# Kernel optimization log

Hardware: AMD Instinct MI355X
Metric: run time of the kernel (lower is better)

## Reference

```python
import jax, jax.numpy as jnp
import numpy as np

NC, NP, H, E, EL = 4096, 8192, 128, 500000, 500000


def setup_inputs() -> dict:
    key = jax.random.key(0)
    ks = jax.random.split(key, 32)
    W = lambda i, shape: jax.random.normal(ks[i], shape, dtype=jnp.float32) * 0.02
    inp = {
        "x_country": jax.random.normal(ks[0], (NC, NC), dtype=jnp.float32),
        "x_product": jax.random.normal(ks[1], (NP, NP), dtype=jnp.float32),
        # input projections (Linear(num_x, hidden)) and node-id embeddings
        "Wc_lin": W(2, (NC, H)), "bc_lin": jnp.zeros((H,), jnp.float32),
        "Wp_lin": W(3, (NP, H)), "bp_lin": jnp.zeros((H,), jnp.float32),
        "emb_c": W(4, (NC, H)),
        "emb_p": W(5, (NP, H)),
        # SAGEConv params per layer per edge type (lin_l has bias, lin_r does not)
        "W1ep_l": W(6, (H, H)), "b1ep": jnp.zeros((H,), jnp.float32), "W1ep_r": W(7, (H, H)),
        "W1pc_l": W(8, (H, H)), "b1pc": jnp.zeros((H,), jnp.float32), "W1pc_r": W(9, (H, H)),
        "W2ep_l": W(10, (H, H)), "b2ep": jnp.zeros((H,), jnp.float32), "W2ep_r": W(11, (H, H)),
        "W2pc_l": W(12, (H, H)), "b2pc": jnp.zeros((H,), jnp.float32), "W2pc_r": W(13, (H, H)),
        # graph structure
        "nid_c": jnp.arange(NC, dtype=jnp.int32),
        "nid_p": jnp.arange(NP, dtype=jnp.int32),
        "e_src": jax.random.randint(ks[14], (E,), 0, NC, dtype=jnp.int32),
        "e_dst": jax.random.randint(ks[15], (E,), 0, NP, dtype=jnp.int32),
        "l_src": jax.random.randint(ks[16], (EL,), 0, NC, dtype=jnp.int32),
        "l_dst": jax.random.randint(ks[17], (EL,), 0, NP, dtype=jnp.int32),
    }
    return inp


def _seg_mean(x, src, dst, n):
    # mean aggregation of source-node features onto destination nodes
    s = jax.ops.segment_sum(x[src], dst, num_segments=n)  # [n, H]
    c = jax.ops.segment_sum(jnp.ones_like(dst, dtype=x.dtype), dst, num_segments=n)
    return s / jnp.maximum(c, 1.0)[:, None]


def _sage(x_src, x_dst, src, dst, Wl, bl, Wr):
    # PyG SAGEConv(mean): lin_l(mean_agg(x_j)) + lin_r(x_i)
    return _seg_mean(x_src, src, dst, x_dst.shape[0]) @ Wl + bl + x_dst @ Wr


def reference(x_country, x_product, Wc_lin, bc_lin, Wp_lin, bp_lin, emb_c, emb_p,
              W1ep_l, b1ep, W1ep_r, W1pc_l, b1pc, W1pc_r,
              W2ep_l, b2ep, W2ep_r, W2pc_l, b2pc, W2pc_r,
              nid_c, nid_p, e_src, e_dst, l_src, l_dst):
    # input fusion: linear(features) + embedding(node_id)
    xc = x_country @ Wc_lin + bc_lin + emb_c[nid_c]  # [NC, H]
    xp = x_product @ Wp_lin + bp_lin + emb_p[nid_p]  # [NP, H]
    # hetero layer 1 (relu per node type); rev edges are the transpose of exports
    hp = jax.nn.relu(_sage(xc, xp, e_src, e_dst, W1ep_l, b1ep, W1ep_r))
    hc = jax.nn.relu(_sage(xp, xc, e_dst, e_src, W1pc_l, b1pc, W1pc_r))
    # hetero layer 2 (no relu)
    hp2 = _sage(hc, hp, e_src, e_dst, W2ep_l, b2ep, W2ep_r)
    hc2 = _sage(hp, hc, e_dst, e_src, W2pc_l, b2pc, W2pc_r)
    # edge-wise dot-product classifier over label edges
    return jnp.sum(hc2[l_src] * hp2[l_dst], axis=-1)  # [EL]
```

## Files before the change

kernel.cpp:

```cpp
#include <hip/hip_runtime.h>
#include <stdint.h>

#define NCn 4096
#define NPn 8192
#define Hn  128
#define En  500000
#define ELn 500000

typedef unsigned short u16;
using f32x4  = __attribute__((ext_vector_type(4))) float;
using bf16x8 = __attribute__((ext_vector_type(8))) short;

__device__ inline u16 f2bf(float f) {
  union { float f; uint32_t u; } v; v.f = f;
  uint32_t r = v.u + 0x7fffu + ((v.u >> 16) & 1u);
  return (u16)(r >> 16);
}

__global__ __launch_bounds__(256) void wtrans(const float* __restrict__ W,
                                              u16* __restrict__ WT, int K) {
  __shared__ float sh[64][33];
  const int k0 = blockIdx.x * 64, n0 = blockIdx.y * 32;
  const int t = threadIdx.x;
  {
    int r = t >> 3, c4 = t & 7;
#pragma unroll
    for (int p = 0; p < 2; ++p) {
      int row = p * 32 + r;
      float4 v = *(const float4*)&W[(size_t)(k0 + row) * 128 + n0 + c4 * 4];
      sh[row][c4 * 4 + 0] = v.x; sh[row][c4 * 4 + 1] = v.y;
      sh[row][c4 * 4 + 2] = v.z; sh[row][c4 * 4 + 3] = v.w;
    }
  }
  __syncthreads();
  int n = t >> 3, kq = t & 7;
  u16 pk[8];
#pragma unroll
  for (int j = 0; j < 8; ++j) pk[j] = f2bf(sh[kq * 8 + j][n]);
  uint4 o;
  o.x = (uint32_t)pk[0] | ((uint32_t)pk[1] << 16);
  o.y = (uint32_t)pk[2] | ((uint32_t)pk[3] << 16);
  o.z = (uint32_t)pk[4] | ((uint32_t)pk[5] << 16);
  o.w = (uint32_t)pk[6] | ((uint32_t)pk[7] << 16);
  *(uint4*)&WT[(size_t)(n0 + n) * K + k0 + kq * 8] = o;
}

__global__ __launch_bounds__(256) void count_deg(const int* __restrict__ esrc,
                                                 const int* __restrict__ edst,
                                                 int* __restrict__ cntC,
                                                 int* __restrict__ cntP) {
  int i = blockIdx.x * 256 + threadIdx.x;
  if (i >= En) return;
  atomicAdd(&cntP[edst[i]], 1);
  atomicAdd(&cntC[esrc[i]], 1);
}

__global__ __launch_bounds__(256) void scan_excl(const int* __restrict__ cnt,
                                                 int* __restrict__ off,
                                                 int* __restrict__ cur, int n) {
  __shared__ int sh[257];
  int t = threadIdx.x;
  int chunk = n >> 8;
  int base = t * chunk;
  int s = 0;
  for (int i = 0; i < chunk; ++i) s += cnt[base + i];
  sh[t] = s;
  __syncthreads();
  if (t == 0) {
    int run = 0;
    for (int i = 0; i < 256; ++i) { int v = sh[i]; sh[i] = run; run += v; }
    sh[256] = run;
  }
  __syncthreads();
  int p = sh[t];
  for (int i = 0; i < chunk; ++i) {
    off[base + i] = p; cur[base + i] = p; p += cnt[base + i];
  }
  if (t == 255) off[n] = sh[256];
}

__global__ __launch_bounds__(256) void fill_adj(const int* __restrict__ esrc,
                                                const int* __restrict__ edst,
                                                int* __restrict__ curC,
                                                int* __restrict__ curP,
                                                int* __restrict__ adjC,
                                                int* __restrict__ adjP) {
  int i = blockIdx.x * 256 + threadIdx.x;
  if (i >= En) return;
  int s = esrc[i], d = edst[i];
  int p = atomicAdd(&curP[d], 1);
  adjP[p] = s;
  int q = atomicAdd(&curC[s], 1);
  adjC[q] = d;
}

__global__ __launch_bounds__(256) void gemm_big_sk(const float* __restrict__ A,
                                                   const u16* __restrict__ BT,
                                                   float* __restrict__ part,
                                                   int K, int Kc) {
  __shared__ __align__(16) u16 aL[64 * 64];
  const int t = threadIdx.x;
  const int wid = t >> 6, lane = t & 63;
  const int ln15 = lane & 15, lhi = lane >> 4;
  const int m0 = blockIdx.x * 64;
  const int kb0 = blockIdx.y * Kc;
  const int nIter = Kc >> 6;
  const size_t M128 = (size_t)gridDim.x * 64 * 128;

  f32x4 acc[4][2] = {};

  const int arow = t >> 2, acq = t & 3;
  const float* Ap = &A[(size_t)(m0 + arow) * K + kb0 + acq * 16];
  const u16* Bp = &BT[(size_t)(wid * 32 + ln15) * K + kb0 + lhi * 8];
  const size_t BniStride = (size_t)16 * K;

#define LOAD_A(dst, koff)                                                      \
  { _Pragma("unroll") for (int i = 0; i < 4; ++i)                              \
      dst[i] = *(const float4*)(Ap + (koff) + i * 4); }
#define LOAD_B(dst, koff)                                                      \
  { _Pragma("unroll") for (int ni = 0; ni < 2; ++ni)                           \
    _Pragma("unroll") for (int ks = 0; ks < 2; ++ks)                           \
      dst[ni][ks] = *(const bf16x8*)(Bp + ni * BniStride + (koff) + ks * 32); }
#define STORE_A_LDS(src)                                                       \
  { u16 pk[16];                                                                \
    _Pragma("unroll") for (int i = 0; i < 4; ++i) {                            \
      pk[i*4+0] = f2bf(src[i].x); pk[i*4+1] = f2bf(src[i].y);                  \
      pk[i*4+2] = f2bf(src[i].z); pk[i*4+3] = f2bf(src[i].w); }                \
    uint4 w0, w1;                                                              \
    w0.x = (uint32_t)pk[0] | ((uint32_t)pk[1] << 16);                          \
    w0.y = (uint32_t)pk[2] | ((uint32_t)pk[3] << 16);                          \
    w0.z = (uint32_t)pk[4] | ((uint32_t)pk[5] << 16);                          \
    w0.w = (uint32_t)pk[6] | ((uint32_t)pk[7] << 16);                          \
    w1.x = (uint32_t)pk[8] | ((uint32_t)pk[9] << 16);                          \
    w1.y = (uint32_t)pk[10] | ((uint32_t)pk[11] << 16);                        \
    w1.z = (uint32_t)pk[12] | ((uint32_t)pk[13] << 16);                        \
    w1.w = (uint32_t)pk[14] | ((uint32_t)pk[15] << 16);                        \
    int sb = arow * 128;                                                       \
    int sw = (arow & 7) << 4;                                                  \
    *(uint4*)((char*)aL + sb + ((acq * 32) ^ sw)) = w0;                        \
    *(uint4*)((char*)aL + sb + ((acq * 32 + 16) ^ sw)) = w1; }
#define COMPUTE(bset)                                                          \
  { _Pragma("unroll") for (int ks = 0; ks < 2; ++ks) {                         \
      bf16x8 afr[4];                                                           \
      _Pragma("unroll") for (int mi = 0; mi < 4; ++mi) {                       \
        int r = mi * 16 + ln15;                                                \
        afr[mi] = *(const bf16x8*)((const char*)aL + r * 128 +                 \
                    ((ks * 64 + lhi * 16) ^ ((r & 7) << 4)));                  \
      }                                                                        \
      _Pragma("unroll") for (int mi = 0; mi < 4; ++mi)                         \
      _Pragma("unroll") for (int ni = 0; ni < 2; ++ni)                         \
        acc[mi][ni] = __builtin_amdgcn_mfma_f32_16x16x32_bf16(                 \
            afr[mi], bset[ni][ks], acc[mi][ni], 0, 0, 0);                      \
    } }

  float4 avA[4], avB[4];
  bf16x8 bvA[2][2], bvB[2][2];
  LOAD_A(avA, 0)
  LOAD_B(bvA, 0)

  for (int it = 0; it < nIter; it += 2) {
    __syncthreads();
    STORE_A_LDS(avA)
    {
      int ko = (it + 1) * 64;
      LOAD_A(avB, ko)
      LOAD_B(bvB, ko)
    }
    __syncthreads();
    COMPUTE(bvA)
    __syncthreads();
    STORE_A_LDS(avB)
    if (it + 2 < nIter) {
      int ko = (it + 2) * 64;
      LOAD_A(avA, ko)
      LOAD_B(bvA, ko)
    }
    __syncthreads();
    COMPUTE(bvB)
  }

  float* P = part + (size_t)blockIdx.y * M128;
#pragma unroll
  for (int mi = 0; mi < 4; ++mi) {
#pragma unroll
    for (int ni = 0; ni < 2; ++ni) {
      int col = wid * 32 + ni * 16 + ln15;
#pragma unroll
      for (int r = 0; r < 4; ++r) {
        int row = m0 + mi * 16 + lhi * 4 + r;
        P[(size_t)row * 128 + col] = acc[mi][ni][r];
      }
    }
  }
#undef LOAD_A
#undef LOAD_B
#undef STORE_A_LDS
#undef COMPUTE
}

__global__ __launch_bounds__(256) void gemm_combine(const float* __restrict__ part,
                                                    const float* __restrict__ bias,
                                                    const float* __restrict__ addend,
                                                    float* __restrict__ out,
                                                    int M, int SK) {
  int i = blockIdx.x * 256 + threadIdx.x;
  int n4 = M * 32;
  if (i >= n4) return;
  size_t stride = (size_t)M * 128;
  f32x4 s = {};
  for (int c = 0; c < SK; ++c) s += *(const f32x4*)&part[c * stride + (size_t)i * 4];
  int col = (i * 4) & 127;
  f32x4 b = *(const f32x4*)&bias[col];
  f32x4 ad = *(const f32x4*)&addend[(size_t)i * 4];
  f32x4 r = s + b + ad;
  *(f32x4*)&out[(size_t)i * 4] = r;
}

template <int RELU>
__global__ __launch_bounds__(256) void gemm_layer(const float* __restrict__ A1,
                                                  const float* __restrict__ A2,
                                                  const float* __restrict__ Wl,
                                                  const float* __restrict__ Wr,
                                                  const float* __restrict__ bias,
                                                  float* __restrict__ out) {
  __shared__ float aT[32][33];
  __shared__ float wT[32][128];
  const int t = threadIdx.x;
  const int tx = t & 15, ty = t >> 4;
  const int m0 = blockIdx.x * 32;
  const int arow = t >> 3, ac = t & 7;
  const int wrow8 = t >> 5, wc = t & 31;
  float acc[2][8] = {};

  float4 a_v;
  float4 w_v[4];
  a_v = *(const float4*)&A1[(size_t)(m0 + arow) * 128 + ac * 4];
#pragma unroll
  for (int i = 0; i < 4; ++i)
    w_v[i] = *(const float4*)&Wl[(size_t)(i * 8 + wrow8) * 128 + wc * 4];

  for (int kc = 0; kc < 8; ++kc) {
    __syncthreads();
    aT[arow][ac * 4 + 0] = a_v.x; aT[arow][ac * 4 + 1] = a_v.y;
    aT[arow][ac * 4 + 2] = a_v.z; aT[arow][ac * 4 + 3] = a_v.w;
#pragma unroll
    for (int i = 0; i < 4; ++i) *(float4*)&wT[i * 8 + wrow8][wc * 4] = w_v[i];
    if (kc + 1 < 8) {
      int nk = kc + 1;
      const float* Asrc = (nk < 4) ? A1 : A2;
      const float* Wsrc = (nk < 4) ? Wl : Wr;
      int kb = (nk & 3) * 32;
      a_v = *(const float4*)&Asrc[(size_t)(m0 + arow) * 128 + kb + ac * 4];
#pragma unroll
      for (int i = 0; i < 4; ++i)
        w_v[i] = *(const float4*)&Wsrc[(size_t)(kb + i * 8 + wrow8) * 128 + wc * 4];
    }
    __syncthreads();
#pragma unroll
    for (int k = 0; k < 32; ++k) {
      float a0 = aT[ty * 2 + 0][k], a1 = aT[ty * 2 + 1][k];
      float4 w0 = *(const float4*)&wT[k][tx * 8];
      float4 w1 = *(const float4*)&wT[k][tx * 8 + 4];
      float w[8] = {w0.x, w0.y, w0.z, w0.w, w1.x, w1.y, w1.z, w1.w};
#pragma unroll
      for (int j = 0; j < 8; ++j) {
        acc[0][j] += a0 * w[j];
        acc[1][j] += a1 * w[j];
      }
    }
  }
#pragma unroll
  for (int i = 0; i < 2; ++i) {
    int row = m0 + ty * 2 + i;
    float o[8];
#pragma unroll
    for (int j = 0; j < 8; ++j) {
      float v = acc[i][j] + bias[tx * 8 + j];
      o[j] = RELU ? fmaxf(v, 0.f) : v;
    }
    float4 v0 = {o[0], o[1], o[2], o[3]}, v1 = {o[4], o[5], o[6], o[7]};
    *(float4*)&out[(size_t)row * 128 + tx * 8] = v0;
    *(float4*)&out[(size_t)row * 128 + tx * 8 + 4] = v1;
  }
}

__global__ __launch_bounds__(256) void agg_mean(const int* __restrict__ adj,
                                                const int* __restrict__ off,
                                                const float* __restrict__ X,
                                                float* __restrict__ out, int ndst) {
  int w = blockIdx.x * 4 + (threadIdx.x >> 6);
  if (w >= ndst) return;
  int lane = threadIdx.x & 63;
  int h = lane >> 5, c = lane & 31;
  int s0 = off[w], deg = off[w + 1] - s0;
  f32x4 acc0 = {}, acc1 = {};
  for (int base = 0; base < deg; base += 64) {
    int my = base + lane;
    int sv = (my < deg) ? adj[s0 + my] : 0;
    int cnt = min(64, deg - base);
    int jj = 0;
    for (; jj + 4 <= cnt; jj += 4) {
      int n0 = __shfl(sv, jj + h);
      int n1 = __shfl(sv, jj + 2 + h);
      f32x4 f0 = *(const f32x4*)&X[(size_t)n0 * 128 + c * 4];
      f32x4 f1 = *(const f32x4*)&X[(size_t)n1 * 128 + c * 4];
      acc0 += f0; acc1 += f1;
    }
    for (; jj < cnt; jj += 2) {
      int idx = jj + h;
      int n = __shfl(sv, min(idx, cnt - 1));
      if (idx < cnt) {
        f32x4 f = *(const f32x4*)&X[(size_t)n * 128 + c * 4];
        acc0 += f;
      }
    }
  }
  f32x4 acc = acc0 + acc1;
#pragma unroll
  for (int j = 0; j < 4; ++j) acc[j] += __shfl_xor(acc[j], 32);
  if (h == 0) {
    float inv = 1.f / (float)max(deg, 1);
    acc *= inv;
    *(f32x4*)&out[(size_t)w * 128 + c * 4] = acc;
  }
}

__global__ __launch_bounds__(256) void edge_dot(const int* __restrict__ ls,
                                                const int* __restrict__ ld,
                                                const float* __restrict__ hc2,
                                                const float* __restrict__ hp2,
                                                float* __restrict__ o, int n) {
  int w = blockIdx.x * 4 + (threadIdx.x >> 6);
  int lane = threadIdx.x & 63;
  int h = lane >> 5, c = lane & 31;
  int e = w * 2 + h;
  if (e >= n) return;
  int s = ls[e], d = ld[e];
  f32x4 a = *(const f32x4*)&hc2[(size_t)s * 128 + c * 4];
  f32x4 b = *(const f32x4*)&hp2[(size_t)d * 128 + c * 4];
  float p = a[0] * b[0] + a[1] * b[1] + a[2] * b[2] + a[3] * b[3];
#pragma unroll
  for (int m = 16; m; m >>= 1) p += __shfl_xor(p, m);
  if (c == 0) o[e] = p;
}

extern "C" void kernel_launch(void* const* d_in, const int* in_sizes, int n_in,
                              void* d_out, int out_size, void* d_ws, size_t ws_size,
                              hipStream_t stream) {
  const float* x_c    = (const float*)d_in[0];
  const float* x_p    = (const float*)d_in[1];
  const float* Wc     = (const float*)d_in[2];
  const float* bc     = (const float*)d_in[3];
  const float* Wp     = (const float*)d_in[4];
  const float* bp     = (const float*)d_in[5];
  const float* emb_c  = (const float*)d_in[6];
  const float* emb_p  = (const float*)d_in[7];
  const float* W1ep_l = (const float*)d_in[8];
  const float* b1ep   = (const float*)d_in[9];
  const float* W1ep_r = (const float*)d_in[10];
  const float* W1pc_l = (const float*)d_in[11];
  const float* b1pc   = (const float*)d_in[12];
  const float* W1pc_r = (const float*)d_in[13];
  const float* W2ep_l = (const float*)d_in[14];
  const float* b2ep   = (const float*)d_in[15];
  const float* W2ep_r = (const float*)d_in[16];
  const float* W2pc_l = (const float*)d_in[17];
  const float* b2pc   = (const float*)d_in[18];
  const float* W2pc_r = (const float*)d_in[19];
  const int* e_src    = (const int*)d_in[22];
  const int* e_dst    = (const int*)d_in[23];
  const int* l_src    = (const int*)d_in[24];
  const int* l_dst    = (const int*)d_in[25];

  size_t off = 0;
  auto alloc = [&](size_t bytes) -> void* {
    void* p = (char*)d_ws + off;
    off += (bytes + 255) & ~(size_t)255;
    return p;
  };
  float* xc    = (float*)alloc((size_t)NCn * Hn * 4);
  float* xp    = (float*)alloc((size_t)NPn * Hn * 4);
  float* aggP  = (float*)alloc((size_t)NPn * Hn * 4);
  float* aggC  = (float*)alloc((size_t)NCn * Hn * 4);
  float* hp    = (float*)alloc((size_t)NPn * Hn * 4);
  float* hc    = (float*)alloc((size_t)NCn * Hn * 4);
  float* hp2   = (float*)alloc((size_t)NPn * Hn * 4);
  float* hc2   = (float*)alloc((size_t)NCn * Hn * 4);
  u16*   WcT   = (u16*)alloc((size_t)Hn * NCn * 2);
  u16*   WpT   = (u16*)alloc((size_t)Hn * NPn * 2);
  float* partP = (float*)alloc((size_t)8 * NPn * Hn * 4);
  float* partC = (float*)alloc((size_t)4 * NCn * Hn * 4);
  int*   adjP  = (int*)alloc((size_t)En * 4);
  int*   adjC  = (int*)alloc((size_t)En * 4);
  int*   offP  = (int*)alloc((size_t)(NPn + 1) * 4);
  int*   offC  = (int*)alloc((size_t)(NCn + 1) * 4);
  int*   curP  = (int*)alloc((size_t)NPn * 4);
  int*   curC  = (int*)alloc((size_t)NCn * 4);
  int*   cnts  = (int*)alloc((size_t)(NPn + NCn) * 4);
  int*   cntP  = cnts;
  int*   cntC  = cnts + NPn;

  hipMemsetAsync(cnts, 0, (size_t)(NPn + NCn) * 4, stream);

  wtrans<<<dim3(NCn / 64, 4), 256, 0, stream>>>(Wc, WcT, NCn);
  wtrans<<<dim3(NPn / 64, 4), 256, 0, stream>>>(Wp, WpT, NPn);

  count_deg<<<(En + 255) / 256, 256, 0, stream>>>(e_src, e_dst, cntC, cntP);
  scan_excl<<<1, 256, 0, stream>>>(cntP, offP, curP, NPn);
  scan_excl<<<1, 256, 0, stream>>>(cntC, offC, curC, NCn);
  fill_adj<<<(En + 255) / 256, 256, 0, stream>>>(e_src, e_dst, curC, curP, adjC, adjP);

  gemm_big_sk<<<dim3(NCn / 64, 4), 256, 0, stream>>>(x_c, WcT, partC, NCn, NCn / 4);
  gemm_big_sk<<<dim3(NPn / 64, 8), 256, 0, stream>>>(x_p, WpT, partP, NPn, NPn / 8);
  gemm_combine<<<(NCn * 32 + 255) / 256, 256, 0, stream>>>(partC, bc, emb_c, xc, NCn, 4);
  gemm_combine<<<(NPn * 32 + 255) / 256, 256, 0, stream>>>(partP, bp, emb_p, xp, NPn, 8);

  agg_mean<<<NPn / 4, 256, 0, stream>>>(adjP, offP, xc, aggP, NPn);
  agg_mean<<<NCn / 4, 256, 0, stream>>>(adjC, offC, xp, aggC, NCn);
  gemm_layer<1><<<NPn / 32, 256, 0, stream>>>(aggP, xp, W1ep_l, W1ep_r, b1ep, hp);
  gemm_layer<1><<<NCn / 32, 256, 0, stream>>>(aggC, xc, W1pc_l, W1pc_r, b1pc, hc);

  agg_mean<<<NPn / 4, 256, 0, stream>>>(adjP, offP, hc, aggP, NPn);
  agg_mean<<<NCn / 4, 256, 0, stream>>>(adjC, offC, hp, aggC, NCn);
  gemm_layer<0><<<NPn / 32, 256, 0, stream>>>(aggP, hp, W2ep_l, W2ep_r, b2ep, hp2);
  gemm_layer<0><<<NCn / 32, 256, 0, stream>>>(aggC, hc, W2pc_l, W2pc_r, b2pc, hc2);

  edge_dot<<<(ELn + 7) / 8, 256, 0, stream>>>(l_src, l_dst, hc2, hp2, (float*)d_out, ELn);
}
```

Before: 882.9 us.

## Gather bf16 copies of node features in mean aggregation, widen edge_dot

The GEMM epilogues now also write bf16 copies of xc/xp/hp/hc, and the mean-aggregation kernel gathers those half-size rows (16 lanes per row, 4 neighbours per wave step) instead of fp32 rows. This halves the bytes moved by the random-access gather over 500k edges, at the cost of bf16 rounding in the aggregated features and extra bf16 stores. edge_dot now handles 4 edges per wave with 8 floats per lane, the two scans merge into one two-block launch, and graph construction is reordered ahead of the weight transposes.

Result: faster. 842.4 us (-4.6%).

```diff
diff --git a/kernel.cpp b/kernel.cpp
--- a/kernel.cpp
+++ b/kernel.cpp
@@ -15,6 +15,9 @@
   union { float f; uint32_t u; } v; v.f = f;
   uint32_t r = v.u + 0x7fffu + ((v.u >> 16) & 1u);
   return (u16)(r >> 16);
+}
+__device__ inline float bfu(uint32_t u) {
+  union { uint32_t x; float f; } z; z.x = u << 16; return z.f;
 }
 
 __global__ __launch_bounds__(256) void wtrans(const float* __restrict__ W,
@@ -55,14 +58,21 @@
   atomicAdd(&cntC[esrc[i]], 1);
 }
 
-__global__ __launch_bounds__(256) void scan_excl(const int* __restrict__ cnt,
-                                                 int* __restrict__ off,
-                                                 int* __restrict__ cur, int n) {
+__global__ __launch_bounds__(256) void scan2(const int* __restrict__ cntP,
+                                             const int* __restrict__ cntC,
+                                             int* __restrict__ offP,
+                                             int* __restrict__ offC,
+                                             int* __restrict__ curP,
+                                             int* __restrict__ curC) {
   __shared__ int sh[257];
+  const int* cnt; int* off; int* cur; int n;
+  if (blockIdx.x == 0) { cnt = cntP; off = offP; cur = curP; n = NPn; }
+  else                 { cnt = cntC; off = offC; cur = curC; n = NCn; }
   int t = threadIdx.x;
   int chunk = n >> 8;
   int base = t * chunk;
   int s = 0;
+#pragma unroll 4
   for (int i = 0; i < chunk; ++i) s += cnt[base + i];
   sh[t] = s;
   __syncthreads();
@@ -202,6 +212,7 @@
                                                     const float* __restrict__ bias,
                                                     const float* __restrict__ addend,
                                                     float* __restrict__ out,
+                                                    u16* __restrict__ outH,
                                                     int M, int SK) {
   int i = blockIdx.x * 256 + threadIdx.x;
   int n4 = M * 32;
@@ -214,6 +225,10 @@
   f32x4 ad = *(const f32x4*)&addend[(size_t)i * 4];
   f32x4 r = s + b + ad;
   *(f32x4*)&out[(size_t)i * 4] = r;
+  uint2 h;
+  h.x = (uint32_t)f2bf(r[0]) | ((uint32_t)f2bf(r[1]) << 16);
+  h.y = (uint32_t)f2bf(r[2]) | ((uint32_t)f2bf(r[3]) << 16);
+  *(uint2*)&outH[(size_t)i * 4] = h;
 }
 
 template <int RELU>
@@ -222,7 +237,8 @@
                                                   const float* __restrict__ Wl,
                                                   const float* __restrict__ Wr,
                                                   const float* __restrict__ bias,
-                                                  float* __restrict__ out) {
+                                                  float* __restrict__ out,
+                                                  u16* __restrict__ outH) {
   __shared__ float aT[32][33];
   __shared__ float wT[32][128];
   const int t = threadIdx.x;
@@ -281,47 +297,72 @@
     float4 v0 = {o[0], o[1], o[2], o[3]}, v1 = {o[4], o[5], o[6], o[7]};
     *(float4*)&out[(size_t)row * 128 + tx * 8] = v0;
     *(float4*)&out[(size_t)row * 128 + tx * 8 + 4] = v1;
-  }
-}
-
-__global__ __launch_bounds__(256) void agg_mean(const int* __restrict__ adj,
-                                                const int* __restrict__ off,
-                                                const float* __restrict__ X,
-                                                float* __restrict__ out, int ndst) {
+    if (outH) {
+      uint4 h;
+      h.x = (uint32_t)f2bf(o[0]) | ((uint32_t)f2bf(o[1]) << 16);
+      h.y = (uint32_t)f2bf(o[2]) | ((uint32_t)f2bf(o[3]) << 16);
+      h.z = (uint32_t)f2bf(o[4]) | ((uint32_t)f2bf(o[5]) << 16);
+      h.w = (uint32_t)f2bf(o[6]) | ((uint32_t)f2bf(o[7]) << 16);
+      *(uint4*)&outH[(size_t)row * 128 + tx * 8] = h;
+    }
+  }
+}
+
+__global__ __launch_bounds__(256) void agg_mean_h(const int* __restrict__ adj,
+                                                  const int* __restrict__ off,
+                                                  const u16* __restrict__ Xh,
+                                                  float* __restrict__ out, int ndst) {
   int w = blockIdx.x * 4 + (threadIdx.x >> 6);
   if (w >= ndst) return;
   int lane = threadIdx.x & 63;
-  int h = lane >> 5, c = lane & 31;
+  int q = lane >> 4, c = lane & 15;
   int s0 = off[w], deg = off[w + 1] - s0;
   f32x4 acc0 = {}, acc1 = {};
+#define ACC8(v)                                                                \
+  { acc0[0] += bfu((v).x & 0xffffu); acc0[1] += bfu((v).x >> 16);              \
+    acc0[2] += bfu((v).y & 0xffffu); acc0[3] += bfu((v).y >> 16);              \
+    acc1[0] += bfu((v).z & 0xffffu); acc1[1] += bfu((v).z >> 16);              \
+    acc1[2] += bfu((v).w & 0xffffu); acc1[3] += bfu((v).w >> 16); }
   for (int base = 0; base < deg; base += 64) {
     int my = base + lane;
     int sv = (my < deg) ? adj[s0 + my] : 0;
     int cnt = min(64, deg - base);
     int jj = 0;
+    for (; jj + 8 <= cnt; jj += 8) {
+      int n0 = __shfl(sv, jj + q);
+      int n1 = __shfl(sv, jj + 4 + q);
+      uint4 v0 = *(const uint4*)&Xh[(size_t)n0 * 128 + c * 8];
+      uint4 v1 = *(const uint4*)&Xh[(size_t)n1 * 128 + c * 8];
+      ACC8(v0)
+      ACC8(v1)
+    }
     for (; jj + 4 <= cnt; jj += 4) {
-      int n0 = __shfl(sv, jj + h);
-      int n1 = __shfl(sv, jj + 2 + h);
-      f32x4 f0 = *(const f32x4*)&X[(size_t)n0 * 128 + c * 4];
-      f32x4 f1 = *(const f32x4*)&X[(size_t)n1 * 128 + c * 4];
-      acc0 += f0; acc1 += f1;
-    }
-    for (; jj < cnt; jj += 2) {
-      int idx = jj + h;
-      int n = __shfl(sv, min(idx, cnt - 1));
-      if (idx < cnt) {
-        f32x4 f = *(const f32x4*)&X[(size_t)n * 128 + c * 4];
-        acc0 += f;
+      int n0 = __shfl(sv, jj + q);
+      uint4 v0 = *(const uint4*)&Xh[(size_t)n0 * 128 + c * 8];
+      ACC8(v0)
+    }
+    int r = cnt - jj;
+    if (r > 0) {
+      int n0 = __shfl(sv, min(jj + q, cnt - 1));
+      if (q < r) {
+        uint4 v0 = *(const uint4*)&Xh[(size_t)n0 * 128 + c * 8];
+        ACC8(v0)
       }
     }
   }
-  f32x4 acc = acc0 + acc1;
-#pragma unroll
-  for (int j = 0; j < 4; ++j) acc[j] += __shfl_xor(acc[j], 32);
-  if (h == 0) {
+#undef ACC8
+#pragma unroll
+  for (int j = 0; j < 4; ++j) {
+    acc0[j] += __shfl_xor(acc0[j], 16);
+    acc0[j] += __shfl_xor(acc0[j], 32);
+    acc1[j] += __shfl_xor(acc1[j], 16);
+    acc1[j] += __shfl_xor(acc1[j], 32);
+  }
+  if (q == 0) {
     float inv = 1.f / (float)max(deg, 1);
-    acc *= inv;
-    *(f32x4*)&out[(size_t)w * 128 + c * 4] = acc;
+    acc0 *= inv; acc1 *= inv;
+    *(f32x4*)&out[(size_t)w * 128 + c * 8] = acc0;
+    *(f32x4*)&out[(size_t)w * 128 + c * 8 + 4] = acc1;
   }
 }
 
@@ -332,15 +373,18 @@
                                                 float* __restrict__ o, int n) {
   int w = blockIdx.x * 4 + (threadIdx.x >> 6);
   int lane = threadIdx.x & 63;
-  int h = lane >> 5, c = lane & 31;
-  int e = w * 2 + h;
+  int q = lane >> 4, c = lane & 15;
+  int e = w * 4 + q;
   if (e >= n) return;
   int s = ls[e], d = ld[e];
-  f32x4 a = *(const f32x4*)&hc2[(size_t)s * 128 + c * 4];
-  f32x4 b = *(const f32x4*)&hp2[(size_t)d * 128 + c * 4];
-  float p = a[0] * b[0] + a[1] * b[1] + a[2] * b[2] + a[3] * b[3];
-#pragma unroll
-  for (int m = 16; m; m >>= 1) p += __shfl_xor(p, m);
+  const float* pa = &hc2[(size_t)s * 128 + c * 8];
+  const float* pb = &hp2[(size_t)d * 128 + c * 8];
+  f32x4 a0 = *(const f32x4*)pa, a1 = *(const f32x4*)(pa + 4);
+  f32x4 b0 = *(const f32x4*)pb, b1 = *(const f32x4*)(pb + 4);
+  f32x4 pv = a0 * b0 + a1 * b1;
+  float p = pv[0] + pv[1] + pv[2] + pv[3];
+#pragma unroll
+  for (int m = 8; m; m >>= 1) p += __shfl_xor(p, m);
   if (c == 0) o[e] = p;
 }
 
@@ -386,6 +430,10 @@
   float* hc    = (float*)alloc((size_t)NCn * Hn * 4);
   float* hp2   = (float*)alloc((size_t)NPn * Hn * 4);
   float* hc2   = (float*)alloc((size_t)NCn * Hn * 4);
+  u16*   xcH   = (u16*)alloc((size_t)NCn * Hn * 2);
+  u16*   xpH   = (u16*)alloc((size_t)NPn * Hn * 2);
+  u16*   hpH   = (u16*)alloc((size_t)NPn * Hn * 2);
+  u16*   hcH   = (u16*)alloc((size_t)NCn * Hn * 2);
   u16*   WcT   = (u16*)alloc((size_t)Hn * NCn * 2);
   u16*   WpT   = (u16*)alloc((size_t)Hn * NPn * 2);
   float* partP = (float*)alloc((size_t)8 * NPn * Hn * 4);
@@ -402,28 +450,27 @@
 
   hipMemsetAsync(cnts, 0, (size_t)(NPn + NCn) * 4, stream);
 
+  count_deg<<<(En + 255) / 256, 256, 0, stream>>>(e_src, e_dst, cntC, cntP);
+  scan2<<<2, 256, 0, stream>>>(cntP, cntC, offP, offC, curP, curC);
+  fill_adj<<<(En + 255) / 256, 256, 0, stream>>>(e_src, e_dst, curC, curP, adjC, adjP);
+
   wtrans<<<dim3(NCn / 64, 4), 256, 0, stream>>>(Wc, WcT, NCn);
   wtrans<<<dim3(NPn / 64, 4), 256, 0, stream>>>(Wp, WpT, NPn);
-
-  count_deg<<<(En + 255) / 256, 256, 0, stream>>>(e_src, e_dst, cntC, cntP);
-  scan_excl<<<1, 256, 0, stream>>>(cntP, offP, curP, NPn);
-  scan_excl<<<1, 256, 0, stream>>>(cntC, offC, curC, NCn);
-  fill_adj<<<(En + 255) / 256, 256, 0, stream>>>(e_src, e_dst, curC, curP, adjC, adjP);
-
   gemm_big_sk<<<dim3(NCn / 64, 4), 256, 0, stream>>>(x_c, WcT, partC, NCn, NCn / 4);
   gemm_big_sk<<<dim3(NPn / 64, 8), 256, 0, stream>>>(x_p, WpT, partP, NPn, NPn / 8);
-  gemm_combine<<<(NCn * 32 + 255) / 256, 256, 0, stream>>>(partC, bc, emb_c, xc, NCn, 4);
-  gemm_combine<<<(NPn * 32 + 255) / 256, 256, 0, stream>>>(partP, bp, emb_p, xp, NPn, 8);
-
-  agg_mean<<<NPn / 4, 256, 0, stream>>>(adjP, offP, xc, aggP, NPn);
-  agg_mean<<<NCn / 4, 256, 0, stream>>>(adjC, offC, xp, aggC, NCn);
-  gemm_layer<1><<<NPn / 32, 256, 0, stream>>>(aggP, xp, W1ep_l, W1ep_r, b1ep, hp);
-  gemm_layer<1><<<NCn / 32, 256, 0, stream>>>(aggC, xc, W1pc_l, W1pc_r, b1pc, hc);
-
-  agg_mean<<<NPn / 4, 256, 0, stream>>>(adjP, offP, hc, aggP, NPn);
-  agg_mean<<<NCn / 4, 256, 0, stream>>>(adjC, offC, hp, aggC, NCn);
-  gemm_layer<0><<<NPn / 32, 256, 0, stream>>>(aggP, hp, W2ep_l, W2ep_r, b2ep, hp2);
-  gemm_layer<0><<<NCn / 32, 256, 0, stream>>>(aggC, hc, W2pc_l, W2pc_r, b2pc, hc2);
-
-  edge_dot<<<(ELn + 7) / 8, 256, 0, stream>>>(l_src, l_dst, hc2, hp2, (float*)d_out, ELn);
-}
+  gemm_combine<<<(NCn * 32 + 255) / 256, 256, 0, stream>>>(partC, bc, emb_c, xc, xcH, NCn, 4);
+  gemm_combine<<<(NPn * 32 + 255) / 256, 256, 0, stream>>>(partP, bp, emb_p, xp, xpH, NPn, 8);
+
+  agg_mean_h<<<NPn / 4, 256, 0, stream>>>(adjP, offP, xcH, aggP, NPn);
+  agg_mean_h<<<NCn / 4, 256, 0, stream>>>(adjC, offC, xpH, aggC, NCn);
+  gemm_layer<1><<<NPn / 32, 256, 0, stream>>>(aggP, xp, W1ep_l, W1ep_r, b1ep, hp, hpH);
+  gemm_layer<1><<<NCn / 32, 256, 0, stream>>>(aggC, xc, W1pc_l, W1pc_r, b1pc, hc, hcH);
+
+  agg_mean_h<<<NPn / 4, 256, 0, stream>>>(adjP, offP, hcH, aggP, NPn);
+  agg_mean_h<<<NCn / 4, 256, 0, stream>>>(adjC, offC, hpH, aggC, NCn);
+  gemm_layer<0><<<NPn / 32, 256, 0, stream>>>(aggP, hp, W2ep_l, W2ep_r, b2ep, hp2, nullptr);
+  gemm_layer<0><<<NCn / 32, 256, 0, stream>>>(aggC, hc, W2pc_l, W2pc_r, b2pc, hc2, nullptr);
+
+  edge_dot<<<(ELn + 15) / 16, 256, 0, stream>>>(l_src, l_dst, hc2, hp2,
+                                                (float*)d_out, ELn);
+}
```
